# Kernel tuning notes

Measured on AMD Instinct MI355X. Metric: run time of the kernel, lower is better.

Reference implementation:

```python
import jax, jax.numpy as jnp
import numpy as np

N_NODES = 50000
N_EDGES = 600000
D = 128
LN_EPS = 1e-5


def setup_inputs() -> dict:
    key = jax.random.key(0)
    ks = jax.random.split(key, 10)
    s = 1.0 / np.sqrt(D)
    return {
        "node_reps": jax.random.normal(ks[0], (N_NODES, D), jnp.float32),
        "edge_reps": jax.random.normal(ks[1], (N_EDGES, D), jnp.float32),
        "src_idx": jax.random.randint(ks[2], (N_EDGES,), 0, N_NODES, jnp.int32),
        "dst_idx": jnp.sort(jax.random.randint(ks[3], (N_EDGES,), 0, N_NODES, jnp.int32)),
        "Wq": jax.random.normal(ks[4], (D, D), jnp.float32) * s,
        "Wk": jax.random.normal(ks[5], (D, D), jnp.float32) * s,
        "Wv": jax.random.normal(ks[6], (D, D), jnp.float32) * s,
        "Wo": jax.random.normal(ks[7], (D, D), jnp.float32) * s,
        "ln_gamma": jnp.ones((D,), jnp.float32),
        "ln_beta": jnp.zeros((D,), jnp.float32),
        "W1": jax.random.normal(ks[8], (3 * D, D), jnp.float32) * (1.0 / np.sqrt(3 * D)),
        "b1": jnp.zeros((D,), jnp.float32),
        "W2": jax.random.normal(ks[9], (D, D), jnp.float32) * s,
        "b2": jnp.zeros((D,), jnp.float32),
    }


def _layer_norm(x, g, b):
    mu = jnp.mean(x, axis=-1, keepdims=True)
    var = jnp.mean(jnp.square(x - mu), axis=-1, keepdims=True)
    return (x - mu) * jax.lax.rsqrt(var + LN_EPS) * g + b


def reference(node_reps, edge_reps, src_idx, dst_idx, Wq, Wk, Wv, Wo,
              ln_gamma, ln_beta, W1, b1, W2, b2):
    n_nodes, d = node_reps.shape
    # dense projections once per node (kernel-friendly GEMMs)
    q = node_reps @ Wq                                  # [N, d]
    k_nodes = node_reps @ Wk                            # [N, d]
    v_nodes = node_reps @ Wv                            # [N, d]
    # per-edge gather + edge bias
    k_e = k_nodes[src_idx] + edge_reps                  # [E, d]
    scores = jnp.sum(q[dst_idx] * k_e, axis=-1) / jnp.sqrt(jnp.float32(d))  # [E]
    # segment softmax over edges sharing the same dst node
    seg_max = jax.ops.segment_max(scores, dst_idx, num_segments=n_nodes)
    ex = jnp.exp(scores - seg_max[dst_idx])
    denom = jax.ops.segment_sum(ex, dst_idx, num_segments=n_nodes)
    alpha = ex / denom[dst_idx]                          # [E]
    v_e = v_nodes[src_idx] + edge_reps                   # [E, d]
    agg = jax.ops.segment_sum(alpha[:, None] * v_e, dst_idx, num_segments=n_nodes)  # [N, d]
    updated = _layer_norm(node_reps + agg @ Wo, ln_gamma, ln_beta)  # [N, d]
    # triplet fusion MLP over (dst node, edge, src node)
    h_trip = jnp.concatenate([node_reps[dst_idx], edge_reps, node_reps[src_idx]], axis=-1)  # [E, 3d]
    fused = jax.nn.relu(h_trip @ W1 + b1) @ W2 + b2      # [E, d]
    return updated, fused
```

## Files before the change

### kernel.cpp

```cpp
#include <hip/hip_runtime.h>
#include <hip/hip_bf16.h>

#define NN 50000
#define NE 600000
#define D 128

typedef __bf16 bf16x8 __attribute__((ext_vector_type(8)));
typedef __bf16 bf16x4 __attribute__((ext_vector_type(4)));
typedef float f32x4 __attribute__((ext_vector_type(4)));

#define MFMA(a, b, c) __builtin_amdgcn_mfma_f32_16x16x32_bf16((a), (b), (c), 0, 0, 0)


static __device__ __forceinline__ void gload_lds16(const void* g, void* l) {
  __builtin_amdgcn_global_load_lds(
      (const __attribute__((address_space(1))) unsigned int*)g,
      (__attribute__((address_space(3))) unsigned int*)l, 16, 0, 0);
}

static __device__ __forceinline__ void stage_a_tile64(const float* __restrict__ A, int M,
                                                      int row_base, char* lds, int tid) {
  const int l32 = tid & 31;
  const int g = tid >> 5;
#pragma unroll
  for (int it = 0; it < 8; ++it) {
    int rl = it * 8 + g;
    int r = row_base + rl;
    f32x4 v = {};
    if (r < M) v = *(const f32x4*)(A + (size_t)r * D + l32 * 4);
    bf16x4 b;
    b[0] = (__bf16)v[0]; b[1] = (__bf16)v[1]; b[2] = (__bf16)v[2]; b[3] = (__bf16)v[3];
    int byte = (rl * 256 + l32 * 8) ^ ((rl & 7) << 4);
    *(bf16x4*)(lds + byte) = b;
  }
}

static __device__ __forceinline__ void stage_a_tile128(const float* __restrict__ A, int M,
                                                       int row_base, char* lds, int tid) {
  const int l32 = tid & 31;
  const int g = tid >> 5;
#pragma unroll
  for (int it = 0; it < 16; ++it) {
    int rl = it * 8 + g;
    int r = row_base + rl;
    f32x4 v = {};
    if (r < M) v = *(const f32x4*)(A + (size_t)r * D + l32 * 4);
    bf16x4 b;
    b[0] = (__bf16)v[0]; b[1] = (__bf16)v[1]; b[2] = (__bf16)v[2]; b[3] = (__bf16)v[3];
    int byte = (rl * 256 + l32 * 8) ^ ((rl & 7) << 4);
    *(bf16x4*)(lds + byte) = b;
  }
}

static __device__ __forceinline__ bf16x8 read_a_frag(const char* lds, int rl, int k0) {
  int byte = (rl * 256 + k0 * 2) ^ ((rl & 7) << 4);
  return *(const bf16x8*)(lds + byte);
}

template <int CTRL>
static __device__ __forceinline__ float dpp_add(float x) {
  int v = __builtin_amdgcn_update_dpp(0, __float_as_int(x), CTRL, 0xf, 0xf, true);
  return x + __int_as_float(v);
}

static __device__ __forceinline__ float red32(float x) {
  x = dpp_add<0xB1>(x);
  x = dpp_add<0x4E>(x);
  x = dpp_add<0x124>(x);
  x = dpp_add<0x128>(x);
  return x + __shfl_xor(x, 16, 64);
}

#define CATT 0.12751744612764933f

struct PrepArgs {
  const float* W[8];
  __bf16* WT[8];
  const int* dst;
  int* offs;
};

__global__ void prep_all(PrepArgs pa) {
  int b = blockIdx.x;
  if (b < 512) {
    int w = b >> 6;
    int t = (b & 63) * 256 + threadIdx.x;
    int n = t & 127, k = t >> 7;
    float v = pa.W[w][k * 128 + n];
    if (w == 0) v *= CATT;
    pa.WT[w][n * 128 + k] = (__bf16)v;
  } else {
    int n = (b - 512) * 256 + threadIdx.x;
    if (n > NN) return;
    int lo = 0, hi = NE;
    while (lo < hi) {
      int mid = (lo + hi) >> 1;
      if (pa.dst[mid] < n) lo = mid + 1; else hi = mid;
    }
    pa.offs[n] = lo;
  }
}

struct GemmBatch {
  const __bf16* BT[5];
  void* C[5];
  const float* bias[5];
  int mode[5];
};

__global__ __launch_bounds__(256) void gemm_k128_b(const float* __restrict__ A,
                                                   GemmBatch gb, int M) {
  __shared__ __align__(16) char atile[128 * 256];
  const int y = blockIdx.y;
  const __bf16* __restrict__ BT = gb.BT[y];
  const int tid = threadIdx.x;
  const int lane = tid & 63;
  const int wave = tid >> 6;
  const int wr = wave >> 1, wc = wave & 1;
  const int row0 = blockIdx.x * 128;
  const int col0 = wc * 64;
  const int lr = lane & 15;
  const int lk = (lane >> 4) << 3;

  stage_a_tile128(A, M, row0, atile, tid);
  __syncthreads();

  f32x4 acc[4][4] = {};
#pragma unroll
  for (int kk = 0; kk < 4; ++kk) {
    const int k0 = kk * 32 + lk;
    bf16x8 a[4], b[4];
#pragma unroll
    for (int m = 0; m < 4; ++m) a[m] = read_a_frag(atile, wr * 64 + m * 16 + lr, k0);
#pragma unroll
    for (int n = 0; n < 4; ++n) b[n] = *(const bf16x8*)(BT + (size_t)(col0 + n * 16 + lr) * D + k0);
#pragma unroll
    for (int m = 0; m < 4; ++m)
#pragma unroll
      for (int n = 0; n < 4; ++n)
        acc[m][n] = MFMA(a[m], b[n], acc[m][n]);
  }
  const int rr = (lane >> 4) * 4;
  float bv[4] = {0.f, 0.f, 0.f, 0.f};
  if (gb.bias[y]) {
#pragma unroll
    for (int n = 0; n < 4; ++n) bv[n] = gb.bias[y][col0 + n * 16 + lr];
  }
  const int mode = gb.mode[y];
#pragma unroll
  for (int m = 0; m < 4; ++m)
#pragma unroll
    for (int j = 0; j < 4; ++j) {
      const int row = row0 + wr * 64 + m * 16 + rr + j;
      if (row < M) {
#pragma unroll
        for (int n = 0; n < 4; ++n) {
          const int c = col0 + n * 16 + lr;
          const float val = acc[m][n][j] + bv[n];
          if (mode == 0) {
            ((float*)gb.C[y])[(size_t)row * D + c] = val;
          } else if (mode == 1) {
            ((__bf16*)gb.C[y])[(size_t)row * D + c] = (__bf16)val;
          } else {
            const int e = ((c >> 2) << 3) + (c & 3) + (mode == 3 ? 4 : 0);
            ((__bf16*)gb.C[y])[(size_t)row * 256 + e] = (__bf16)val;
          }
        }
      }
    }
}

__global__ __launch_bounds__(256) void edge_mlp(
    const float* __restrict__ edge,
    const __bf16* __restrict__ W1bT,
    const __bf16* __restrict__ W2T,
    const __bf16* __restrict__ P1,
    const __bf16* __restrict__ P3,
    const int* __restrict__ dst,
    const int* __restrict__ src,
    const float* __restrict__ b2,
    float* __restrict__ out_fused) {
  __shared__ __align__(16) char atile[64 * 256];
  __shared__ __align__(16) char bufP3[64 * 256];
  const int tid = threadIdx.x;
  const int swz = (blockIdx.x & 7) * 1172 + (blockIdx.x >> 3);
  if (swz >= NE / 64) return;
  const int eb = swz * 64;
  const int lane = tid & 63;
  const int wave = tid >> 6;
  const int wr = wave >> 1, wc = wave & 1;
  const int lr = lane & 15;
  const int lk = (lane >> 4) << 3;
  const int col0 = wc * 64;
  const int rr = (lane >> 4) * 4;

  {
    const int gr = lane >> 4;
    const int slot = lane & 15;
    int sg[4];
#pragma unroll
    for (int c = 0; c < 4; ++c) sg[c] = src[eb + wave * 16 + c * 4 + gr];
#pragma unroll
    for (int c = 0; c < 4; ++c) {
      int rl = wave * 16 + c * 4 + gr;
      int sb = (slot * 16) ^ ((rl & 7) << 4);
      gload_lds16((const char*)(P3 + (size_t)sg[c] * D) + sb,
                  bufP3 + (wave * 16 + c * 4) * 256);
    }
  }

  stage_a_tile64(edge, NE, eb, atile, tid);
  __syncthreads();

  f32x4 acc[2][4] = {};
#pragma unroll
  for (int kk = 0; kk < 4; ++kk) {
    const int k0 = kk * 32 + lk;
    bf16x8 a[2], bm[4];
#pragma unroll
    for (int m = 0; m < 2; ++m) a[m] = read_a_frag(atile, wr * 32 + m * 16 + lr, k0);
#pragma unroll
    for (int n = 0; n < 4; ++n) bm[n] = *(const bf16x8*)(W1bT + (size_t)(col0 + n * 16 + lr) * D + k0);
#pragma unroll
    for (int m = 0; m < 2; ++m)
#pragma unroll
      for (int n = 0; n < 4; ++n)
        acc[m][n] = MFMA(a[m], bm[n], acc[m][n]);
  }
  __syncthreads();

#pragma unroll
  for (int m = 0; m < 2; ++m) {
#pragma unroll
    for (int j = 0; j < 4; ++j) {
      const int rl = wr * 32 + m * 16 + rr + j;
      const __bf16* __restrict__ p1r = P1 + (size_t)dst[eb + rl] * D;
#pragma unroll
      for (int n = 0; n < 4; ++n) {
        const int c = col0 + n * 16 + lr;
        int byte = (rl * 256 + c * 2) ^ ((rl & 7) << 4);
        float g3 = (float)*(const __bf16*)(bufP3 + byte);
        float v = fmaxf(acc[m][n][j] + (float)p1r[c] + g3, 0.f);
        *(__bf16*)(atile + byte) = (__bf16)v;
      }
    }
  }
  __syncthreads();

  float b2v[4];
#pragma unroll
  for (int n = 0; n < 4; ++n) b2v[n] = b2[col0 + n * 16 + lr];
  f32x4 acc2[2][4] = {};
#pragma unroll
  for (int kk = 0; kk < 4; ++kk) {
    const int k0 = kk * 32 + lk;
    bf16x8 a[2], bm[4];
#pragma unroll
    for (int m = 0; m < 2; ++m) a[m] = read_a_frag(atile, wr * 32 + m * 16 + lr, k0);
#pragma unroll
    for (int n = 0; n < 4; ++n) bm[n] = *(const bf16x8*)(W2T + (size_t)(col0 + n * 16 + lr) * D + k0);
#pragma unroll
    for (int m = 0; m < 2; ++m)
#pragma unroll
      for (int n = 0; n < 4; ++n)
        acc2[m][n] = MFMA(a[m], bm[n], acc2[m][n]);
  }
#pragma unroll
  for (int m = 0; m < 2; ++m)
#pragma unroll
    for (int j = 0; j < 4; ++j) {
      int rl = wr * 32 + m * 16 + rr + j;
      int e = eb + rl;
#pragma unroll
      for (int n = 0; n < 4; ++n) {
        int c = col0 + n * 16 + lr;
        out_fused[(size_t)e * D + c] = acc2[m][n][j] + b2v[n];
      }
    }
}

#define LD1(P, K, J, SV)                                                     \
  do {                                                                       \
    const int jj_ = (J);                                                     \
    const int jc_ = jj_ < jm ? jj_ : 0;                                      \
    int si_ = __shfl((SV), jj_ & 31, 32);                                    \
    si_ = jj_ < jm ? si_ : 0;                                                \
    kv##P[K] = *(const bf16x8*)(KV + (size_t)si_ * 256 + (l32 << 3));        \
    ee##P[K] = *(const f32x4*)(edge + (size_t)(s0 + jc_) * D + (l32 << 2));  \
  } while (0)

#define LOADC(P, C)                                                          \
  do {                                                                       \
    const int c4_ = (C) * 4;                                                 \
    const int sv_ = (c4_ < 32) ? sidx0 : sidx1;                              \
    LD1(P, 0, c4_ + 0, sv_); LD1(P, 1, c4_ + 1, sv_);                        \
    LD1(P, 2, c4_ + 2, sv_); LD1(P, 3, c4_ + 3, sv_);                        \
  } while (0)

#define CP1(P, K, J)                                                         \
  do {                                                                       \
    const int jj_ = (J);                                                     \
    f32x4 ef_ = ee##P[K];                                                    \
    float x0_ = (float)kv##P[K][0] + ef_[0];                                 \
    float x1_ = (float)kv##P[K][1] + ef_[1];                                 \
    float x2_ = (float)kv##P[K][2] + ef_[2];                                 \
    float x3_ = (float)kv##P[K][3] + ef_[3];                                 \
    float pp_ = fmaf(qs[1], x1_, qs[0] * x0_) + fmaf(qs[3], x3_, qs[2] * x2_); \
    float s_ = red32(pp_);                                                   \
    float w_ = jj_ < jm ? exp2f(s_) : 0.f;                                   \
    l += w_;                                                                 \
    a[0] = fmaf(w_, (float)kv##P[K][4] + ef_[0], a[0]);                      \
    a[1] = fmaf(w_, (float)kv##P[K][5] + ef_[1], a[1]);                      \
    a[2] = fmaf(w_, (float)kv##P[K][6] + ef_[2], a[2]);                      \
    a[3] = fmaf(w_, (float)kv##P[K][7] + ef_[3], a[3]);                      \
  } while (0)

#define COMPC(P, C)                                                          \
  do {                                                                       \
    const int cc4_ = (C) * 4;                                                \
    CP1(P, 0, cc4_ + 0); CP1(P, 1, cc4_ + 1);                                \
    CP1(P, 2, cc4_ + 2); CP1(P, 3, cc4_ + 3);                                \
  } while (0)

__global__ __launch_bounds__(256) __attribute__((amdgpu_waves_per_eu(3)))
void attn_node(
    const float* __restrict__ edge,
    const int* __restrict__ src,
    const float* __restrict__ Q,
    const __bf16* __restrict__ KV,
    const int* __restrict__ offs,
    const __bf16* __restrict__ WoT,
    const float* __restrict__ noderep,
    const float* __restrict__ gamma,
    const float* __restrict__ beta,
    float* __restrict__ out_updated) {
  __shared__ __align__(16) char buf[8192];
  const int tid = threadIdx.x;
  const int nw = tid >> 5;
  const int node = blockIdx.x * 8 + nw;
  const int l32 = tid & 31;
  int s0 = offs[node], s1 = offs[node + 1];
  int cnt = s1 - s0;
  f32x4 qs = *(const f32x4*)(Q + (size_t)node * D + l32 * 4);
  float l = 0.f;
  f32x4 a = {0.f, 0.f, 0.f, 0.f};

  const int jm = cnt < 64 ? cnt : 64;
  if (jm > 0) {
    int sidx0 = 0, sidx1 = 0;
    if (l32 < cnt) sidx0 = src[s0 + l32];
    if (l32 + 32 < cnt) sidx1 = src[s0 + 32 + l32];
    bf16x8 kv0[4], kv1[4];
    f32x4 ee0[4], ee1[4];
    const int nch = (jm + 3) >> 2;
    LOADC(0, 0);
    for (int c = 0; c < nch; c += 2) {
      if (c + 1 < nch) LOADC(1, c + 1);
      COMPC(0, c);
      if (c + 2 < nch) LOADC(0, c + 2);
      if (c + 1 < nch) COMPC(1, c + 1);
    }
    for (int i = 64; i < cnt; ++i) {
      int si = src[s0 + i];
      bf16x8 kvx = *(const bf16x8*)(KV + (size_t)si * 256 + (l32 << 3));
      f32x4 ef = *(const f32x4*)(edge + (size_t)(s0 + i) * D + (l32 << 2));
      float x0 = (float)kvx[0] + ef[0], x1 = (float)kvx[1] + ef[1];
      float x2 = (float)kvx[2] + ef[2], x3 = (float)kvx[3] + ef[3];
      float pp = fmaf(qs[1], x1, qs[0] * x0) + fmaf(qs[3], x3, qs[2] * x2);
      float w = exp2f(red32(pp));
      l += w;
      a[0] = fmaf(w, (float)kvx[4] + ef[0], a[0]);
      a[1] = fmaf(w, (float)kvx[5] + ef[1], a[1]);
      a[2] = fmaf(w, (float)kvx[6] + ef[2], a[2]);
      a[3] = fmaf(w, (float)kvx[7] + ef[3], a[3]);
    }
  }
  float inv = l > 0.f ? 1.f / l : 0.f;
  f32x4 r;
  r[0] = a[0] * inv; r[1] = a[1] * inv; r[2] = a[2] * inv; r[3] = a[3] * inv;

  {
    bf16x4 rb;
    rb[0] = (__bf16)r[0]; rb[1] = (__bf16)r[1];
    rb[2] = (__bf16)r[2]; rb[3] = (__bf16)r[3];
    int byte = (nw * 256 + l32 * 8) ^ ((nw & 7) << 4);
    *(bf16x4*)(buf + byte) = rb;
  }
  __syncthreads();

  {
    const int wave = tid >> 6;
    const int lane = tid & 63;
    const int lr = lane & 15;
    const int lk = (lane >> 4) << 3;
    f32x4 acc[2] = {};
#pragma unroll
    for (int kk = 0; kk < 4; ++kk) {
      int k0 = kk * 32 + lk;
      bf16x8 af = read_a_frag(buf, lr, k0);
#pragma unroll
      for (int tt = 0; tt < 2; ++tt) {
        int nn = wave * 2 + tt;
        bf16x8 bm = *(const bf16x8*)(WoT + (size_t)(nn * 16 + lr) * D + k0);
        acc[tt] = MFMA(af, bm, acc[tt]);
      }
    }
    float* xl = (float*)(buf + 4096);
    const int rr = (lane >> 4) * 4;
    if (rr < 8) {
#pragma unroll
      for (int tt = 0; tt < 2; ++tt) {
        int nn = wave * 2 + tt;
#pragma unroll
        for (int j = 0; j < 4; ++j)
          xl[(rr + j) * 128 + nn * 16 + lr] = acc[tt][j];
      }
    }
  }
  __syncthreads();

  {
    const float* xl = (const float*)(buf + 4096);
    f32x4 xv = *(const f32x4*)(xl + nw * 128 + l32 * 4);
    f32x4 nv = *(const f32x4*)(noderep + (size_t)node * D + l32 * 4);
    float x0 = xv[0] + nv[0], x1 = xv[1] + nv[1];
    float x2 = xv[2] + nv[2], x3 = xv[3] + nv[3];
    float s = red32(x0 + x1 + x2 + x3);
    float mu = s * (1.f / 128.f);
    float d0 = x0 - mu, d1 = x1 - mu, d2 = x2 - mu, d3 = x3 - mu;
    float vv = red32(d0 * d0 + d1 * d1 + d2 * d2 + d3 * d3);
    float rstd = rsqrtf(vv * (1.f / 128.f) + 1e-5f);
    f32x4 g = *(const f32x4*)(gamma + l32 * 4);
    f32x4 bb = *(const f32x4*)(beta + l32 * 4);
    f32x4 o;
    o[0] = d0 * rstd * g[0] + bb[0];
    o[1] = d1 * rstd * g[1] + bb[1];
    o[2] = d2 * rstd * g[2] + bb[2];
    o[3] = d3 * rstd * g[3] + bb[3];
    *(f32x4*)(out_updated + (size_t)node * D + l32 * 4) = o;
  }
}

extern "C" void kernel_launch(void* const* d_in, const int* in_sizes, int n_in,
                              void* d_out, int out_size, void* d_ws, size_t ws_size,
                              hipStream_t stream) {
  const float* node = (const float*)d_in[0];
  const float* edge = (const float*)d_in[1];
  const int* src = (const int*)d_in[2];
  const int* dst = (const int*)d_in[3];
  const float* Wq = (const float*)d_in[4];
  const float* Wk = (const float*)d_in[5];
  const float* Wv = (const float*)d_in[6];
  const float* Wo = (const float*)d_in[7];
  const float* gamma = (const float*)d_in[8];
  const float* beta = (const float*)d_in[9];
  const float* W1 = (const float*)d_in[10];
  const float* b1 = (const float*)d_in[11];
  const float* W2 = (const float*)d_in[12];
  const float* b2 = (const float*)d_in[13];

  float* out_updated = (float*)d_out;
  float* out_fused = (float*)d_out + (size_t)NN * D;

  char* ws = (char*)d_ws;
  size_t o = 0;
  auto take = [&](size_t bytes) {
    char* p = ws + o;
    o = (o + bytes + 255) & ~(size_t)255;
    return p;
  };
  int* offs = (int*)take((NN + 1) * sizeof(int));
  __bf16* WqT = (__bf16*)take(128 * 128 * 2);
  __bf16* WkT = (__bf16*)take(128 * 128 * 2);
  __bf16* WvT = (__bf16*)take(128 * 128 * 2);
  __bf16* WoT = (__bf16*)take(128 * 128 * 2);
  __bf16* W1aT = (__bf16*)take(128 * 128 * 2);
  __bf16* W1bT = (__bf16*)take(128 * 128 * 2);
  __bf16* W1cT = (__bf16*)take(128 * 128 * 2);
  __bf16* W2T = (__bf16*)take(128 * 128 * 2);
  float* Qb = (float*)take((size_t)NN * D * 4);
  __bf16* KVb = (__bf16*)take((size_t)NN * 256 * 2);
  __bf16* P1b = (__bf16*)take((size_t)NN * D * 2);
  __bf16* P3b = (__bf16*)take((size_t)NN * D * 2);

  PrepArgs pa;
  pa.W[0] = Wq; pa.WT[0] = WqT;
  pa.W[1] = Wk; pa.WT[1] = WkT;
  pa.W[2] = Wv; pa.WT[2] = WvT;
  pa.W[3] = Wo; pa.WT[3] = WoT;
  pa.W[4] = W1; pa.WT[4] = W1aT;
  pa.W[5] = W1 + 128 * 128; pa.WT[5] = W1bT;
  pa.W[6] = W1 + 256 * 128; pa.WT[6] = W1cT;
  pa.W[7] = W2; pa.WT[7] = W2T;
  pa.dst = dst; pa.offs = offs;
  prep_all<<<512 + (NN + 256) / 256, 256, 0, stream>>>(pa);

  int gnode = (NN + 127) / 128;
  GemmBatch gb;
  gb.BT[0] = WqT;  gb.C[0] = Qb;  gb.bias[0] = nullptr; gb.mode[0] = 0;
  gb.BT[1] = WkT;  gb.C[1] = KVb; gb.bias[1] = nullptr; gb.mode[1] = 2;
  gb.BT[2] = WvT;  gb.C[2] = KVb; gb.bias[2] = nullptr; gb.mode[2] = 3;
  gb.BT[3] = W1aT; gb.C[3] = P1b; gb.bias[3] = b1;      gb.mode[3] = 1;
  gb.BT[4] = W1cT; gb.C[4] = P3b; gb.bias[4] = nullptr; gb.mode[4] = 1;
  gemm_k128_b<<<dim3(gnode, 5), 256, 0, stream>>>(node, gb, NN);

  edge_mlp<<<9376, 256, 0, stream>>>(edge, W1bT, W2T, P1b, P3b, dst, src,
                                     b2, out_fused);
  attn_node<<<NN / 8, 256, 0, stream>>>(edge, src, Qb, KVb, offs,
                                        WoT, node, gamma, beta, out_updated);
}
```

Before: 442.5 us.

## Merge edge MLP and node attention kernels into one role-dispatched launch

Replaces the separate edge_mlp and attn_node launches with a single kernel. Each group of blocks is split into two attention roles (8 nodes each) and three edge-MLP roles (64 edges each), so both workloads interleave on the GPU and share one tail. This removes a launch boundary and lets the compute-heavy MFMA blocks overlap with the gather-bound attention blocks. In exchange, the attention path now reserves the larger 32 KB shared allocation and runs under the waves-per-eu attribute, which may lower occupancy for those blocks.

```diff
diff --git a/kernel.cpp b/kernel.cpp
--- a/kernel.cpp
+++ b/kernel.cpp
@@ -166,115 +166,6 @@
             ((__bf16*)gb.C[y])[(size_t)row * 256 + e] = (__bf16)val;
           }
         }
-      }
-    }
-}
-
-__global__ __launch_bounds__(256) void edge_mlp(
-    const float* __restrict__ edge,
-    const __bf16* __restrict__ W1bT,
-    const __bf16* __restrict__ W2T,
-    const __bf16* __restrict__ P1,
-    const __bf16* __restrict__ P3,
-    const int* __restrict__ dst,
-    const int* __restrict__ src,
-    const float* __restrict__ b2,
-    float* __restrict__ out_fused) {
-  __shared__ __align__(16) char atile[64 * 256];
-  __shared__ __align__(16) char bufP3[64 * 256];
-  const int tid = threadIdx.x;
-  const int swz = (blockIdx.x & 7) * 1172 + (blockIdx.x >> 3);
-  if (swz >= NE / 64) return;
-  const int eb = swz * 64;
-  const int lane = tid & 63;
-  const int wave = tid >> 6;
-  const int wr = wave >> 1, wc = wave & 1;
-  const int lr = lane & 15;
-  const int lk = (lane >> 4) << 3;
-  const int col0 = wc * 64;
-  const int rr = (lane >> 4) * 4;
-
-  {
-    const int gr = lane >> 4;
-    const int slot = lane & 15;
-    int sg[4];
-#pragma unroll
-    for (int c = 0; c < 4; ++c) sg[c] = src[eb + wave * 16 + c * 4 + gr];
-#pragma unroll
-    for (int c = 0; c < 4; ++c) {
-      int rl = wave * 16 + c * 4 + gr;
-      int sb = (slot * 16) ^ ((rl & 7) << 4);
-      gload_lds16((const char*)(P3 + (size_t)sg[c] * D) + sb,
-                  bufP3 + (wave * 16 + c * 4) * 256);
-    }
-  }
-
-  stage_a_tile64(edge, NE, eb, atile, tid);
-  __syncthreads();
-
-  f32x4 acc[2][4] = {};
-#pragma unroll
-  for (int kk = 0; kk < 4; ++kk) {
-    const int k0 = kk * 32 + lk;
-    bf16x8 a[2], bm[4];
-#pragma unroll
-    for (int m = 0; m < 2; ++m) a[m] = read_a_frag(atile, wr * 32 + m * 16 + lr, k0);
-#pragma unroll
-    for (int n = 0; n < 4; ++n) bm[n] = *(const bf16x8*)(W1bT + (size_t)(col0 + n * 16 + lr) * D + k0);
-#pragma unroll
-    for (int m = 0; m < 2; ++m)
-#pragma unroll
-      for (int n = 0; n < 4; ++n)
-        acc[m][n] = MFMA(a[m], bm[n], acc[m][n]);
-  }
-  __syncthreads();
-
-#pragma unroll
-  for (int m = 0; m < 2; ++m) {
-#pragma unroll
-    for (int j = 0; j < 4; ++j) {
-      const int rl = wr * 32 + m * 16 + rr + j;
-      const __bf16* __restrict__ p1r = P1 + (size_t)dst[eb + rl] * D;
-#pragma unroll
-      for (int n = 0; n < 4; ++n) {
-        const int c = col0 + n * 16 + lr;
-        int byte = (rl * 256 + c * 2) ^ ((rl & 7) << 4);
-        float g3 = (float)*(const __bf16*)(bufP3 + byte);
-        float v = fmaxf(acc[m][n][j] + (float)p1r[c] + g3, 0.f);
-        *(__bf16*)(atile + byte) = (__bf16)v;
-      }
-    }
-  }
-  __syncthreads();
-
-  float b2v[4];
-#pragma unroll
-  for (int n = 0; n < 4; ++n) b2v[n] = b2[col0 + n * 16 + lr];
-  f32x4 acc2[2][4] = {};
-#pragma unroll
-  for (int kk = 0; kk < 4; ++kk) {
-    const int k0 = kk * 32 + lk;
-    bf16x8 a[2], bm[4];
-#pragma unroll
-    for (int m = 0; m < 2; ++m) a[m] = read_a_frag(atile, wr * 32 + m * 16 + lr, k0);
-#pragma unroll
-    for (int n = 0; n < 4; ++n) bm[n] = *(const bf16x8*)(W2T + (size_t)(col0 + n * 16 + lr) * D + k0);
-#pragma unroll
-    for (int m = 0; m < 2; ++m)
-#pragma unroll
-      for (int n = 0; n < 4; ++n)
-        acc2[m][n] = MFMA(a[m], bm[n], acc2[m][n]);
-  }
-#pragma unroll
-  for (int m = 0; m < 2; ++m)
-#pragma unroll
-    for (int j = 0; j < 4; ++j) {
-      int rl = wr * 32 + m * 16 + rr + j;
-      int e = eb + rl;
-#pragma unroll
-      for (int n = 0; n < 4; ++n) {
-        int c = col0 + n * 16 + lr;
-        out_fused[(size_t)e * D + c] = acc2[m][n][j] + b2v[n];
       }
     }
 }
@@ -323,9 +214,16 @@
   } while (0)
 
 __global__ __launch_bounds__(256) __attribute__((amdgpu_waves_per_eu(3)))
-void attn_node(
+void fused_edge_attn(
     const float* __restrict__ edge,
+    const __bf16* __restrict__ W1bT,
+    const __bf16* __restrict__ W2T,
+    const __bf16* __restrict__ P1,
+    const __bf16* __restrict__ P3,
+    const int* __restrict__ dst,
     const int* __restrict__ src,
+    const float* __restrict__ b2,
+    float* __restrict__ out_fused,
     const float* __restrict__ Q,
     const __bf16* __restrict__ KV,
     const int* __restrict__ offs,
@@ -334,110 +232,214 @@
     const float* __restrict__ gamma,
     const float* __restrict__ beta,
     float* __restrict__ out_updated) {
-  __shared__ __align__(16) char buf[8192];
+  __shared__ __align__(16) char atile[64 * 256];
+  __shared__ __align__(16) char bufP3[64 * 256];
   const int tid = threadIdx.x;
-  const int nw = tid >> 5;
-  const int node = blockIdx.x * 8 + nw;
-  const int l32 = tid & 31;
-  int s0 = offs[node], s1 = offs[node + 1];
-  int cnt = s1 - s0;
-  f32x4 qs = *(const f32x4*)(Q + (size_t)node * D + l32 * 4);
-  float l = 0.f;
-  f32x4 a = {0.f, 0.f, 0.f, 0.f};
-
-  const int jm = cnt < 64 ? cnt : 64;
-  if (jm > 0) {
-    int sidx0 = 0, sidx1 = 0;
-    if (l32 < cnt) sidx0 = src[s0 + l32];
-    if (l32 + 32 < cnt) sidx1 = src[s0 + 32 + l32];
-    bf16x8 kv0[4], kv1[4];
-    f32x4 ee0[4], ee1[4];
-    const int nch = (jm + 3) >> 2;
-    LOADC(0, 0);
-    for (int c = 0; c < nch; c += 2) {
-      if (c + 1 < nch) LOADC(1, c + 1);
-      COMPC(0, c);
-      if (c + 2 < nch) LOADC(0, c + 2);
-      if (c + 1 < nch) COMPC(1, c + 1);
-    }
-    for (int i = 64; i < cnt; ++i) {
-      int si = src[s0 + i];
-      bf16x8 kvx = *(const bf16x8*)(KV + (size_t)si * 256 + (l32 << 3));
-      f32x4 ef = *(const f32x4*)(edge + (size_t)(s0 + i) * D + (l32 << 2));
-      float x0 = (float)kvx[0] + ef[0], x1 = (float)kvx[1] + ef[1];
-      float x2 = (float)kvx[2] + ef[2], x3 = (float)kvx[3] + ef[3];
-      float pp = fmaf(qs[1], x1, qs[0] * x0) + fmaf(qs[3], x3, qs[2] * x2);
-      float w = exp2f(red32(pp));
-      l += w;
-      a[0] = fmaf(w, (float)kvx[4] + ef[0], a[0]);
-      a[1] = fmaf(w, (float)kvx[5] + ef[1], a[1]);
-      a[2] = fmaf(w, (float)kvx[6] + ef[2], a[2]);
-      a[3] = fmaf(w, (float)kvx[7] + ef[3], a[3]);
-    }
-  }
-  float inv = l > 0.f ? 1.f / l : 0.f;
-  f32x4 r;
-  r[0] = a[0] * inv; r[1] = a[1] * inv; r[2] = a[2] * inv; r[3] = a[3] * inv;
-
-  {
-    bf16x4 rb;
-    rb[0] = (__bf16)r[0]; rb[1] = (__bf16)r[1];
-    rb[2] = (__bf16)r[2]; rb[3] = (__bf16)r[3];
-    int byte = (nw * 256 + l32 * 8) ^ ((nw & 7) << 4);
-    *(bf16x4*)(buf + byte) = rb;
-  }
-  __syncthreads();
-
-  {
+  const int b = blockIdx.x;
+  const int x = b & 7;
+  const int t = b >> 3;
+  const int grp = (t / 5) * 8 + x;
+  const int role = t % 5;
+  if (grp >= 3125) return;
+
+  if (role >= 2) {
+    const int ebi = grp * 3 + (role - 2);
+    const int eb = ebi * 64;
+    const int lane = tid & 63;
     const int wave = tid >> 6;
-    const int lane = tid & 63;
+    const int wr = wave >> 1, wc = wave & 1;
     const int lr = lane & 15;
     const int lk = (lane >> 4) << 3;
-    f32x4 acc[2] = {};
+    const int col0 = wc * 64;
+    const int rr = (lane >> 4) * 4;
+
+    {
+      const int gr = lane >> 4;
+      const int slot = lane & 15;
+      int sg[4];
+#pragma unroll
+      for (int c = 0; c < 4; ++c) sg[c] = src[eb + wave * 16 + c * 4 + gr];
+#pragma unroll
+      for (int c = 0; c < 4; ++c) {
+        int rl = wave * 16 + c * 4 + gr;
+        int sb = (slot * 16) ^ ((rl & 7) << 4);
+        gload_lds16((const char*)(P3 + (size_t)sg[c] * D) + sb,
+                    bufP3 + (wave * 16 + c * 4) * 256);
+      }
+    }
+
+    stage_a_tile64(edge, NE, eb, atile, tid);
+    __syncthreads();
+
+    f32x4 acc[2][4] = {};
 #pragma unroll
     for (int kk = 0; kk < 4; ++kk) {
-      int k0 = kk * 32 + lk;
-      bf16x8 af = read_a_frag(buf, lr, k0);
-#pragma unroll
-      for (int tt = 0; tt < 2; ++tt) {
-        int nn = wave * 2 + tt;
-        bf16x8 bm = *(const bf16x8*)(WoT + (size_t)(nn * 16 + lr) * D + k0);
-        acc[tt] = MFMA(af, bm, acc[tt]);
-      }
-    }
-    float* xl = (float*)(buf + 4096);
-    const int rr = (lane >> 4) * 4;
-    if (rr < 8) {
-#pragma unroll
-      for (int tt = 0; tt < 2; ++tt) {
-        int nn = wave * 2 + tt;
-#pragma unroll
-        for (int j = 0; j < 4; ++j)
-          xl[(rr + j) * 128 + nn * 16 + lr] = acc[tt][j];
-      }
-    }
-  }
-  __syncthreads();
-
-  {
-    const float* xl = (const float*)(buf + 4096);
-    f32x4 xv = *(const f32x4*)(xl + nw * 128 + l32 * 4);
-    f32x4 nv = *(const f32x4*)(noderep + (size_t)node * D + l32 * 4);
-    float x0 = xv[0] + nv[0], x1 = xv[1] + nv[1];
-    float x2 = xv[2] + nv[2], x3 = xv[3] + nv[3];
-    float s = red32(x0 + x1 + x2 + x3);
-    float mu = s * (1.f / 128.f);
-    float d0 = x0 - mu, d1 = x1 - mu, d2 = x2 - mu, d3 = x3 - mu;
-    float vv = red32(d0 * d0 + d1 * d1 + d2 * d2 + d3 * d3);
-    float rstd = rsqrtf(vv * (1.f / 128.f) + 1e-5f);
-    f32x4 g = *(const f32x4*)(gamma + l32 * 4);
-    f32x4 bb = *(const f32x4*)(beta + l32 * 4);
-    f32x4 o;
-    o[0] = d0 * rstd * g[0] + bb[0];
-    o[1] = d1 * rstd * g[1] + bb[1];
-    o[2] = d2 * rstd * g[2] + bb[2];
-    o[3] = d3 * rstd * g[3] + bb[3];
-    *(f32x4*)(out_updated + (size_t)node * D + l32 * 4) = o;
+      const int k0 = kk * 32 + lk;
+      bf16x8 a[2], bm[4];
+#pragma unroll
+      for (int m = 0; m < 2; ++m) a[m] = read_a_frag(atile, wr * 32 + m * 16 + lr, k0);
+#pragma unroll
+      for (int n = 0; n < 4; ++n) bm[n] = *(const bf16x8*)(W1bT + (size_t)(col0 + n * 16 + lr) * D + k0);
+#pragma unroll
+      for (int m = 0; m < 2; ++m)
+#pragma unroll
+        for (int n = 0; n < 4; ++n)
+          acc[m][n] = MFMA(a[m], bm[n], acc[m][n]);
+    }
+    __syncthreads();
+
+#pragma unroll
+    for (int m = 0; m < 2; ++m) {
+#pragma unroll
+      for (int j = 0; j < 4; ++j) {
+        const int rl = wr * 32 + m * 16 + rr + j;
+        const __bf16* __restrict__ p1r = P1 + (size_t)dst[eb + rl] * D;
+#pragma unroll
+        for (int n = 0; n < 4; ++n) {
+          const int c = col0 + n * 16 + lr;
+          int byte = (rl * 256 + c * 2) ^ ((rl & 7) << 4);
+          float g3 = (float)*(const __bf16*)(bufP3 + byte);
+          float v = fmaxf(acc[m][n][j] + (float)p1r[c] + g3, 0.f);
+          *(__bf16*)(atile + byte) = (__bf16)v;
+        }
+      }
+    }
+    __syncthreads();
+
+    float b2v[4];
+#pragma unroll
+    for (int n = 0; n < 4; ++n) b2v[n] = b2[col0 + n * 16 + lr];
+    f32x4 acc2[2][4] = {};
+#pragma unroll
+    for (int kk = 0; kk < 4; ++kk) {
+      const int k0 = kk * 32 + lk;
+      bf16x8 a[2], bm[4];
+#pragma unroll
+      for (int m = 0; m < 2; ++m) a[m] = read_a_frag(atile, wr * 32 + m * 16 + lr, k0);
+#pragma unroll
+      for (int n = 0; n < 4; ++n) bm[n] = *(const bf16x8*)(W2T + (size_t)(col0 + n * 16 + lr) * D + k0);
+#pragma unroll
+      for (int m = 0; m < 2; ++m)
+#pragma unroll
+        for (int n = 0; n < 4; ++n)
+          acc2[m][n] = MFMA(a[m], bm[n], acc2[m][n]);
+    }
+#pragma unroll
+    for (int m = 0; m < 2; ++m)
+#pragma unroll
+      for (int j = 0; j < 4; ++j) {
+        int rl = wr * 32 + m * 16 + rr + j;
+        int e = eb + rl;
+#pragma unroll
+        for (int n = 0; n < 4; ++n) {
+          int c = col0 + n * 16 + lr;
+          out_fused[(size_t)e * D + c] = acc2[m][n][j] + b2v[n];
+        }
+      }
+  } else {
+    const int nw = tid >> 5;
+    const int node = (grp * 2 + role) * 8 + nw;
+    const int l32 = tid & 31;
+    int s0 = offs[node], s1 = offs[node + 1];
+    int cnt = s1 - s0;
+    f32x4 qs = *(const f32x4*)(Q + (size_t)node * D + l32 * 4);
+    float l = 0.f;
+    f32x4 a = {0.f, 0.f, 0.f, 0.f};
+
+    const int jm = cnt < 64 ? cnt : 64;
+    if (jm > 0) {
+      int sidx0 = 0, sidx1 = 0;
+      if (l32 < cnt) sidx0 = src[s0 + l32];
+      if (l32 + 32 < cnt) sidx1 = src[s0 + 32 + l32];
+      bf16x8 kv0[4], kv1[4];
+      f32x4 ee0[4], ee1[4];
+      const int nch = (jm + 3) >> 2;
+      LOADC(0, 0);
+      for (int c = 0; c < nch; c += 2) {
+        if (c + 1 < nch) LOADC(1, c + 1);
+        COMPC(0, c);
+        if (c + 2 < nch) LOADC(0, c + 2);
+        if (c + 1 < nch) COMPC(1, c + 1);
+      }
+      for (int i = 64; i < cnt; ++i) {
+        int si = src[s0 + i];
+        bf16x8 kvx = *(const bf16x8*)(KV + (size_t)si * 256 + (l32 << 3));
+        f32x4 ef = *(const f32x4*)(edge + (size_t)(s0 + i) * D + (l32 << 2));
+        float x0 = (float)kvx[0] + ef[0], x1 = (float)kvx[1] + ef[1];
+        float x2 = (float)kvx[2] + ef[2], x3 = (float)kvx[3] + ef[3];
+        float pp = fmaf(qs[1], x1, qs[0] * x0) + fmaf(qs[3], x3, qs[2] * x2);
+        float w = exp2f(red32(pp));
+        l += w;
+        a[0] = fmaf(w, (float)kvx[4] + ef[0], a[0]);
+        a[1] = fmaf(w, (float)kvx[5] + ef[1], a[1]);
+        a[2] = fmaf(w, (float)kvx[6] + ef[2], a[2]);
+        a[3] = fmaf(w, (float)kvx[7] + ef[3], a[3]);
+      }
+    }
+    float inv = l > 0.f ? 1.f / l : 0.f;
+    f32x4 r;
+    r[0] = a[0] * inv; r[1] = a[1] * inv; r[2] = a[2] * inv; r[3] = a[3] * inv;
+
+    {
+      bf16x4 rb;
+      rb[0] = (__bf16)r[0]; rb[1] = (__bf16)r[1];
+      rb[2] = (__bf16)r[2]; rb[3] = (__bf16)r[3];
+      int byte = (nw * 256 + l32 * 8) ^ ((nw & 7) << 4);
+      *(bf16x4*)(atile + byte) = rb;
+    }
+    __syncthreads();
+
+    {
+      const int wave = tid >> 6;
+      const int lane = tid & 63;
+      const int lr = lane & 15;
+      const int lk = (lane >> 4) << 3;
+      f32x4 acc[2] = {};
+#pragma unroll
+      for (int kk = 0; kk < 4; ++kk) {
+        int k0 = kk * 32 + lk;
+        bf16x8 af = read_a_frag(atile, lr, k0);
+#pragma unroll
+        for (int tt = 0; tt < 2; ++tt) {
+          int nn = wave * 2 + tt;
+          bf16x8 bm = *(const bf16x8*)(WoT + (size_t)(nn * 16 + lr) * D + k0);
+          acc[tt] = MFMA(af, bm, acc[tt]);
+        }
+      }
+      float* xl = (float*)(atile + 4096);
+      const int rr = (lane >> 4) * 4;
+      if (rr < 8) {
+#pragma unroll
+        for (int tt = 0; tt < 2; ++tt) {
+          int nn = wave * 2 + tt;
+#pragma unroll
+          for (int j = 0; j < 4; ++j)
+            xl[(rr + j) * 128 + nn * 16 + lr] = acc[tt][j];
+        }
+      }
+    }
+    __syncthreads();
+
+    {
+      const float* xl = (const float*)(atile + 4096);
+      f32x4 xv = *(const f32x4*)(xl + nw * 128 + l32 * 4);
+      f32x4 nv = *(const f32x4*)(noderep + (size_t)node * D + l32 * 4);
+      float x0 = xv[0] + nv[0], x1 = xv[1] + nv[1];
+      float x2 = xv[2] + nv[2], x3 = xv[3] + nv[3];
+      float s = red32(x0 + x1 + x2 + x3);
+      float mu = s * (1.f / 128.f);
+      float d0 = x0 - mu, d1 = x1 - mu, d2 = x2 - mu, d3 = x3 - mu;
+      float vv = red32(d0 * d0 + d1 * d1 + d2 * d2 + d3 * d3);
+      float rstd = rsqrtf(vv * (1.f / 128.f) + 1e-5f);
+      f32x4 g = *(const f32x4*)(gamma + l32 * 4);
+      f32x4 bb = *(const f32x4*)(beta + l32 * 4);
+      f32x4 o;
+      o[0] = d0 * rstd * g[0] + bb[0];
+      o[1] = d1 * rstd * g[1] + bb[1];
+      o[2] = d2 * rstd * g[2] + bb[2];
+      o[3] = d3 * rstd * g[3] + bb[3];
+      *(f32x4*)(out_updated + (size_t)node * D + l32 * 4) = o;
+    }
   }
 }
 
@@ -504,8 +506,7 @@
   gb.BT[4] = W1cT; gb.C[4] = P3b; gb.bias[4] = nullptr; gb.mode[4] = 1;
   gemm_k128_b<<<dim3(gnode, 5), 256, 0, stream>>>(node, gb, NN);
 
-  edge_mlp<<<9376, 256, 0, stream>>>(edge, W1bT, W2T, P1b, P3b, dst, src,
-                                     b2, out_fused);
-  attn_node<<<NN / 8, 256, 0, stream>>>(edge, src, Qb, KVb, offs,
-                                        WoT, node, gamma, beta, out_updated);
-}
+  fused_edge_attn<<<15640, 256, 0, stream>>>(edge, W1bT, W2T, P1b, P3b, dst, src,
+                                             b2, out_fused, Qb, KVb, offs,
+                                             WoT, node, gamma, beta, out_updated);
+}
```

After: 401.3 us. -9.3%, faster.
